# Performance work log

Hardware: AMD Instinct MI355X
Metric: run time of the kernel (lower is better)

Reference implementation:

```python
import jax, jax.numpy as jnp
import numpy as np

N_NODE = 4096
FMAPS = 64
HIDDEN = 8


def setup_inputs() -> dict:
    key = jax.random.key(0)
    k1, k2, k3, k4, k5, k6 = jax.random.split(key, 6)
    adj_in = jax.random.uniform(k1, (1, N_NODE, N_NODE), dtype=jnp.float32)
    emb_in = jax.random.normal(k2, (1, FMAPS, N_NODE), dtype=jnp.float32)
    # Linear(2*fmaps+1 -> nb_hidden) and Linear(nb_hidden -> 8), torch layout [out, in]
    W1 = jax.random.normal(k3, (HIDDEN, 2 * FMAPS + 1), dtype=jnp.float32) * 0.1
    b1 = jax.random.normal(k4, (HIDDEN,), dtype=jnp.float32) * 0.1
    W2 = jax.random.normal(k5, (8, HIDDEN), dtype=jnp.float32) * 0.1
    b2 = jax.random.normal(k6, (8,), dtype=jnp.float32) * 0.1
    return {"adj_in": adj_in, "emb_in": emb_in, "W1": W1, "b1": b1, "W2": W2, "b2": b2}


def reference(adj_in, emb_in, W1, b1, W2, b2):
    # Original module only supports batch==1 (squeeze + column assign constraint).
    batch, fmap, nb_node = emb_in.shape  # [1, F, N]
    A = adj_in[0]                        # [N, N]
    E = emb_in[0].T                      # [N, F] node embeddings

    # mean incoming edge weight per node k: (column-sum minus self edge) / (N-1)
    sum_w = (jnp.sum(A, axis=0) - jnp.diagonal(A)) / (nb_node - 1)  # [N]

    # Pairwise input for pair (j,k) is [E[j], E[k], sum_w[k]] fed through layer1.
    # Decompose layer1 linearly instead of materializing the [N*N, 2F+1] tensor.
    W1a = W1[:, :fmap]            # acts on first sample (row j)
    W1b = W1[:, fmap:2 * fmap]    # acts on second sample (col k)
    w1c = W1[:, 2 * fmap]         # acts on incoming edge weight (col k)

    aj = E @ W1a.T + b1                               # [N, H] contribution of j
    bk = E @ W1b.T + sum_w[:, None] * w1c[None, :]    # [N, H] contribution of k

    h = jax.nn.relu(aj[:, None, :] + bk[None, :, :])  # [N, N, H]
    # layer2 then keep output channel 0 only (as original scatters edge_out[:, 0])
    adj = h @ W2[0] + b2[0]                           # [N, N]
    return adj[None]                                  # [1, N, N]
```

## Files before the change

kernel.cpp:

```cpp
#include <hip/hip_runtime.h>

#define N 4096
#define F 64
#define H 8
#define PCHUNKS 256
#define W1S (2 * F + 1)

__global__ __launch_bounds__(256) void colsum_partial(const float* __restrict__ A,
                                                      float* __restrict__ partial) {
    int c4 = blockIdx.x * 256 + threadIdx.x;
    int r0 = blockIdx.y * (N / PCHUNKS);
    const float* p = A + (size_t)r0 * N + (size_t)c4 * 4;
    float4 acc = make_float4(0.f, 0.f, 0.f, 0.f);
#pragma unroll
    for (int r = 0; r < N / PCHUNKS; ++r) {
        float4 v = *(const float4*)(p + (size_t)r * N);
        acc.x += v.x; acc.y += v.y; acc.z += v.z; acc.w += v.w;
    }
    *(float4*)(partial + (size_t)blockIdx.y * N + (size_t)c4 * 4) = acc;
}

__global__ __launch_bounds__(256) void fuse_tile(const float* __restrict__ A,
                                                 const float* __restrict__ emb,
                                                 const float* __restrict__ W1,
                                                 const float* __restrict__ b1,
                                                 const float* __restrict__ W2,
                                                 const float* __restrict__ b2,
                                                 const float* __restrict__ partial,
                                                 float* __restrict__ out) {
    __shared__ float ajs[128][12];
    __shared__ float bks_s[128][12];
    __shared__ float psum[128][2];

    const int t  = threadIdx.x;
    const int j0 = blockIdx.x * 128;
    const int i0 = blockIdx.y * 128;

    {
        int c = t & 127;
        int half = t >> 7;
        const float* pp = partial + (size_t)half * 128 * N + (size_t)j0 + c;
        float s = 0.f;
#pragma unroll 16
        for (int p = 0; p < 128; ++p) s += pp[(size_t)p * N];
        psum[c][half] = s;
    }
    __syncthreads();

    if (t < 128) {
        int j = j0 + t;
        float sw = (psum[t][0] + psum[t][1] - A[(size_t)j * N + j]) * (1.0f / (float)(N - 1));
        float b[H];
#pragma unroll
        for (int k = 0; k < H; ++k) b[k] = sw * W1[k * W1S + 2 * F];
#pragma unroll
        for (int f = 0; f < F; ++f) {
            float e = emb[(size_t)f * N + j];
#pragma unroll
            for (int k = 0; k < H; ++k) b[k] += e * W1[k * W1S + F + f];
        }
#pragma unroll
        for (int k = 0; k < H; ++k) bks_s[t][k] = b[k];
    } else {
        int r = t - 128;
        int i = i0 + r;
        float a[H];
#pragma unroll
        for (int k = 0; k < H; ++k) a[k] = b1[k];
#pragma unroll
        for (int f = 0; f < F; ++f) {
            float e = emb[(size_t)f * N + i];
#pragma unroll
            for (int k = 0; k < H; ++k) a[k] += e * W1[k * W1S + f];
        }
#pragma unroll
        for (int k = 0; k < H; ++k) ajs[r][k] = a[k];
    }
    __syncthreads();

    int tx = t & 31;
    int ty = t >> 5;
    int j  = j0 + tx * 4;

    float w2[H];
#pragma unroll
    for (int k = 0; k < H; ++k) w2[k] = W2[k];
    float b20 = b2[0];

    float bkr[4][H];
#pragma unroll
    for (int c = 0; c < 4; ++c) {
        float4 lo = *(const float4*)&bks_s[tx * 4 + c][0];
        float4 hi = *(const float4*)&bks_s[tx * 4 + c][4];
        bkr[c][0] = lo.x; bkr[c][1] = lo.y; bkr[c][2] = lo.z; bkr[c][3] = lo.w;
        bkr[c][4] = hi.x; bkr[c][5] = hi.y; bkr[c][6] = hi.z; bkr[c][7] = hi.w;
    }

#pragma unroll
    for (int r = 0; r < 16; ++r) {
        int row = ty * 16 + r;
        float a[H];
        float4 lo = *(const float4*)&ajs[row][0];
        float4 hi = *(const float4*)&ajs[row][4];
        a[0] = lo.x; a[1] = lo.y; a[2] = lo.z; a[3] = lo.w;
        a[4] = hi.x; a[5] = hi.y; a[6] = hi.z; a[7] = hi.w;

        float res[4];
#pragma unroll
        for (int c = 0; c < 4; ++c) {
            float acc = b20;
#pragma unroll
            for (int k = 0; k < H; ++k) {
                float tt = a[k] + bkr[c][k];
                acc += fmaxf(tt, 0.f) * w2[k];
            }
            res[c] = acc;
        }
        *(float4*)(out + (size_t)(i0 + row) * N + j) = make_float4(res[0], res[1], res[2], res[3]);
    }
}

extern "C" void kernel_launch(void* const* d_in, const int* in_sizes, int n_in,
                              void* d_out, int out_size, void* d_ws, size_t ws_size,
                              hipStream_t stream) {
    const float* adj = (const float*)d_in[0];
    const float* emb = (const float*)d_in[1];
    const float* W1  = (const float*)d_in[2];
    const float* b1  = (const float*)d_in[3];
    const float* W2  = (const float*)d_in[4];
    const float* b2  = (const float*)d_in[5];
    float* out = (float*)d_out;

    float* partial = (float*)d_ws;

    colsum_partial<<<dim3(4, PCHUNKS), 256, 0, stream>>>(adj, partial);
    fuse_tile<<<dim3(N / 128, N / 128), 256, 0, stream>>>(adj, emb, W1, b1, W2, b2,
                                                          partial, out);
}
```

Before: 40.80 us.

## Fuse column-sum and pairwise MLP into one kernel with per-stripe atomic barrier

Merges the column-sum pass into the main kernel. Each block reduces a 256x128 tile of A, writes a partial, then spins on a per-column-stripe atomic counter until all 16 row bands have contributed. Blocks now cover 256 output rows, so the aj projection is computed for two rows per thread. This removes one launch and the 256-chunk partial buffer but adds a memset, a grid-wide spin wait that relies on all 512 blocks being co-resident, and a serialized reduction before any output is written.

```diff
diff --git a/kernel.cpp b/kernel.cpp
--- a/kernel.cpp
+++ b/kernel.cpp
@@ -3,120 +3,145 @@
 #define N 4096
 #define F 64
 #define H 8
-#define PCHUNKS 256
 #define W1S (2 * F + 1)
+#define NSTRIPE 32
+#define NBAND 16
 
-__global__ __launch_bounds__(256) void colsum_partial(const float* __restrict__ A,
-                                                      float* __restrict__ partial) {
-    int c4 = blockIdx.x * 256 + threadIdx.x;
-    int r0 = blockIdx.y * (N / PCHUNKS);
-    const float* p = A + (size_t)r0 * N + (size_t)c4 * 4;
-    float4 acc = make_float4(0.f, 0.f, 0.f, 0.f);
-#pragma unroll
-    for (int r = 0; r < N / PCHUNKS; ++r) {
-        float4 v = *(const float4*)(p + (size_t)r * N);
-        acc.x += v.x; acc.y += v.y; acc.z += v.z; acc.w += v.w;
-    }
-    *(float4*)(partial + (size_t)blockIdx.y * N + (size_t)c4 * 4) = acc;
-}
-
-__global__ __launch_bounds__(256) void fuse_tile(const float* __restrict__ A,
-                                                 const float* __restrict__ emb,
-                                                 const float* __restrict__ W1,
-                                                 const float* __restrict__ b1,
-                                                 const float* __restrict__ W2,
-                                                 const float* __restrict__ b2,
-                                                 const float* __restrict__ partial,
-                                                 float* __restrict__ out) {
-    __shared__ float ajs[128][12];
-    __shared__ float bks_s[128][12];
-    __shared__ float psum[128][2];
+__global__ __launch_bounds__(256, 2) void fused_all(
+    const float* __restrict__ A, const float* __restrict__ emb,
+    const float* __restrict__ W1, const float* __restrict__ b1,
+    const float* __restrict__ W2, const float* __restrict__ b2,
+    unsigned* __restrict__ cnt, float* __restrict__ partial,
+    float* __restrict__ out)
+{
+    __shared__ float4 ps[8][32];
+    __shared__ float ajs[256][12];
+    __shared__ float bks[128][12];
 
     const int t  = threadIdx.x;
-    const int j0 = blockIdx.x * 128;
-    const int i0 = blockIdx.y * 128;
+    const int s  = blockIdx.x >> 4;
+    const int rb = blockIdx.x & 15;
+    const int j0 = s * 128;
+    const int i0 = rb * 256;
 
     {
-        int c = t & 127;
-        int half = t >> 7;
-        const float* pp = partial + (size_t)half * 128 * N + (size_t)j0 + c;
-        float s = 0.f;
+        int c4 = t & 31;
+        int rg = t >> 5;
+        const float* p = A + (size_t)(i0 + rg * 32) * N + j0 + c4 * 4;
+        float4 acc = make_float4(0.f, 0.f, 0.f, 0.f);
 #pragma unroll 16
-        for (int p = 0; p < 128; ++p) s += pp[(size_t)p * N];
-        psum[c][half] = s;
+        for (int r = 0; r < 32; ++r) {
+            float4 v = *(const float4*)(p + (size_t)r * N);
+            acc.x += v.x; acc.y += v.y; acc.z += v.z; acc.w += v.w;
+        }
+        ps[rg][c4] = acc;
+    }
+    __syncthreads();
+    if (t < 32) {
+        float4 tot = make_float4(0.f, 0.f, 0.f, 0.f);
+#pragma unroll
+        for (int g = 0; g < 8; ++g) {
+            float4 v = ps[g][t];
+            tot.x += v.x; tot.y += v.y; tot.z += v.z; tot.w += v.w;
+        }
+        *(float4*)(partial + (size_t)blockIdx.x * 128 + t * 4) = tot;
+    }
+    __syncthreads();
+
+    if (t == 0) {
+        __threadfence();
+        atomicAdd(&cnt[s], 1u);
+        while (__hip_atomic_load(&cnt[s], __ATOMIC_RELAXED,
+                                 __HIP_MEMORY_SCOPE_AGENT) < (unsigned)NBAND) {
+            __builtin_amdgcn_s_sleep(16);
+        }
+        __threadfence();
     }
     __syncthreads();
 
     if (t < 128) {
+        float tot = 0.f;
+#pragma unroll
+        for (int r = 0; r < NBAND; ++r)
+            tot += partial[(size_t)(s * NBAND + r) * 128 + t];
         int j = j0 + t;
-        float sw = (psum[t][0] + psum[t][1] - A[(size_t)j * N + j]) * (1.0f / (float)(N - 1));
-        float b[H];
+        float sw = (tot - A[(size_t)j * N + j]) * (1.0f / (float)(N - 1));
+        float bv[H];
 #pragma unroll
-        for (int k = 0; k < H; ++k) b[k] = sw * W1[k * W1S + 2 * F];
+        for (int k = 0; k < H; ++k) bv[k] = sw * W1[k * W1S + 2 * F];
 #pragma unroll
         for (int f = 0; f < F; ++f) {
             float e = emb[(size_t)f * N + j];
 #pragma unroll
-            for (int k = 0; k < H; ++k) b[k] += e * W1[k * W1S + F + f];
+            for (int k = 0; k < H; ++k) bv[k] += e * W1[k * W1S + F + f];
         }
 #pragma unroll
-        for (int k = 0; k < H; ++k) bks_s[t][k] = b[k];
+        for (int k = 0; k < H; ++k) bks[t][k] = bv[k];
     } else {
-        int r = t - 128;
-        int i = i0 + r;
-        float a[H];
+        int u = t - 128;
+        float a0[H], a1[H];
 #pragma unroll
-        for (int k = 0; k < H; ++k) a[k] = b1[k];
+        for (int k = 0; k < H; ++k) { a0[k] = b1[k]; a1[k] = b1[k]; }
 #pragma unroll
         for (int f = 0; f < F; ++f) {
-            float e = emb[(size_t)f * N + i];
+            float e0 = emb[(size_t)f * N + i0 + u];
+            float e1 = emb[(size_t)f * N + i0 + 128 + u];
 #pragma unroll
-            for (int k = 0; k < H; ++k) a[k] += e * W1[k * W1S + f];
+            for (int k = 0; k < H; ++k) {
+                a0[k] += e0 * W1[k * W1S + f];
+                a1[k] += e1 * W1[k * W1S + f];
+            }
         }
 #pragma unroll
-        for (int k = 0; k < H; ++k) ajs[r][k] = a[k];
+        for (int k = 0; k < H; ++k) { ajs[u][k] = a0[k]; ajs[128 + u][k] = a1[k]; }
     }
     __syncthreads();
 
-    int tx = t & 31;
-    int ty = t >> 5;
-    int j  = j0 + tx * 4;
+    {
+        int tx = t & 31;
+        int ty = t >> 5;
+        int j  = j0 + tx * 4;
 
-    float w2[H];
+        float w2[H];
 #pragma unroll
-    for (int k = 0; k < H; ++k) w2[k] = W2[k];
-    float b20 = b2[0];
+        for (int k = 0; k < H; ++k) w2[k] = W2[k];
+        float b20 = b2[0];
 
-    float bkr[4][H];
-#pragma unroll
-    for (int c = 0; c < 4; ++c) {
-        float4 lo = *(const float4*)&bks_s[tx * 4 + c][0];
-        float4 hi = *(const float4*)&bks_s[tx * 4 + c][4];
-        bkr[c][0] = lo.x; bkr[c][1] = lo.y; bkr[c][2] = lo.z; bkr[c][3] = lo.w;
-        bkr[c][4] = hi.x; bkr[c][5] = hi.y; bkr[c][6] = hi.z; bkr[c][7] = hi.w;
-    }
-
-#pragma unroll
-    for (int r = 0; r < 16; ++r) {
-        int row = ty * 16 + r;
-        float a[H];
-        float4 lo = *(const float4*)&ajs[row][0];
-        float4 hi = *(const float4*)&ajs[row][4];
-        a[0] = lo.x; a[1] = lo.y; a[2] = lo.z; a[3] = lo.w;
-        a[4] = hi.x; a[5] = hi.y; a[6] = hi.z; a[7] = hi.w;
-
-        float res[4];
+        float bkr[4][H];
 #pragma unroll
         for (int c = 0; c < 4; ++c) {
-            float acc = b20;
+            float4 lo = *(const float4*)&bks[tx * 4 + c][0];
+            float4 hi = *(const float4*)&bks[tx * 4 + c][4];
+            bkr[c][0] = lo.x; bkr[c][1] = lo.y; bkr[c][2] = lo.z; bkr[c][3] = lo.w;
+            bkr[c][4] = hi.x; bkr[c][5] = hi.y; bkr[c][6] = hi.z; bkr[c][7] = hi.w;
+        }
+
+#pragma unroll 2
+        for (int half = 0; half < 2; ++half) {
 #pragma unroll
-            for (int k = 0; k < H; ++k) {
-                float tt = a[k] + bkr[c][k];
-                acc += fmaxf(tt, 0.f) * w2[k];
+            for (int r = 0; r < 16; ++r) {
+                int row = half * 128 + ty * 16 + r;
+                float a[H];
+                float4 lo = *(const float4*)&ajs[row][0];
+                float4 hi = *(const float4*)&ajs[row][4];
+                a[0] = lo.x; a[1] = lo.y; a[2] = lo.z; a[3] = lo.w;
+                a[4] = hi.x; a[5] = hi.y; a[6] = hi.z; a[7] = hi.w;
+
+                float res[4];
+#pragma unroll
+                for (int c = 0; c < 4; ++c) {
+                    float acc = b20;
+#pragma unroll
+                    for (int k = 0; k < H; ++k) {
+                        float tt = a[k] + bkr[c][k];
+                        acc += fmaxf(tt, 0.f) * w2[k];
+                    }
+                    res[c] = acc;
+                }
+                *(float4*)(out + (size_t)(i0 + row) * N + j) =
+                    make_float4(res[0], res[1], res[2], res[3]);
             }
-            res[c] = acc;
         }
-        *(float4*)(out + (size_t)(i0 + row) * N + j) = make_float4(res[0], res[1], res[2], res[3]);
     }
 }
 
@@ -131,9 +156,10 @@
     const float* b2  = (const float*)d_in[5];
     float* out = (float*)d_out;
 
-    float* partial = (float*)d_ws;
+    unsigned* cnt  = (unsigned*)d_ws;
+    float* partial = (float*)((char*)d_ws + 512);
 
-    colsum_partial<<<dim3(4, PCHUNKS), 256, 0, stream>>>(adj, partial);
-    fuse_tile<<<dim3(N / 128, N / 128), 256, 0, stream>>>(adj, emb, W1, b1, W2, b2,
-                                                          partial, out);
+    hipMemsetAsync(d_ws, 0, 512, stream);
+    fused_all<<<dim3(NSTRIPE * NBAND), 256, 0, stream>>>(adj, emb, W1, b1, W2, b2,
+                                                         cnt, partial, out);
 }
```

New measurement: 90.22 us. 2.21x slower.

## Widen output tile to 256 columns and halve column-sum partial chunks

Applied to the files above, without the earlier changes.

The column-sum pre-pass now uses 128 row chunks of 32 rows instead of 256 chunks of 16, which halves the partial buffer each tile must re-read. The main kernel tile grows to 128x256, so every thread computes one column's bk vector directly from its own partial sum, without the shared-memory reduction and its extra barrier. Each thread also writes 32 rows instead of 16. This cuts redundant per-tile recomputation of bk and aj and the partial-sum rereads, at the cost of fewer blocks and more per-thread serial work.

```diff
diff --git a/kernel.cpp b/kernel.cpp
--- a/kernel.cpp
+++ b/kernel.cpp
@@ -3,17 +3,17 @@
 #define N 4096
 #define F 64
 #define H 8
-#define PCHUNKS 256
 #define W1S (2 * F + 1)
+#define PCH 128
 
 __global__ __launch_bounds__(256) void colsum_partial(const float* __restrict__ A,
                                                       float* __restrict__ partial) {
     int c4 = blockIdx.x * 256 + threadIdx.x;
-    int r0 = blockIdx.y * (N / PCHUNKS);
+    int r0 = blockIdx.y * 32;
     const float* p = A + (size_t)r0 * N + (size_t)c4 * 4;
     float4 acc = make_float4(0.f, 0.f, 0.f, 0.f);
-#pragma unroll
-    for (int r = 0; r < N / PCHUNKS; ++r) {
+#pragma unroll 16
+    for (int r = 0; r < 32; ++r) {
         float4 v = *(const float4*)(p + (size_t)r * N);
         acc.x += v.x; acc.y += v.y; acc.z += v.z; acc.w += v.w;
     }
@@ -29,57 +29,53 @@
                                                  const float* __restrict__ partial,
                                                  float* __restrict__ out) {
     __shared__ float ajs[128][12];
-    __shared__ float bks_s[128][12];
-    __shared__ float psum[128][2];
+    __shared__ float bks[256][12];
 
     const int t  = threadIdx.x;
-    const int j0 = blockIdx.x * 128;
+    const int j0 = blockIdx.x * 256;
     const int i0 = blockIdx.y * 128;
 
+    float s = 0.f;
     {
-        int c = t & 127;
-        int half = t >> 7;
-        const float* pp = partial + (size_t)half * 128 * N + (size_t)j0 + c;
-        float s = 0.f;
+        const float* pp = partial + j0 + t;
 #pragma unroll 16
-        for (int p = 0; p < 128; ++p) s += pp[(size_t)p * N];
-        psum[c][half] = s;
+        for (int p = 0; p < PCH; ++p) s += pp[(size_t)p * N];
     }
-    __syncthreads();
 
-    if (t < 128) {
+    {
         int j = j0 + t;
-        float sw = (psum[t][0] + psum[t][1] - A[(size_t)j * N + j]) * (1.0f / (float)(N - 1));
-        float b[H];
+        float sw = (s - A[(size_t)j * N + j]) * (1.0f / (float)(N - 1));
+        float bv[H];
 #pragma unroll
-        for (int k = 0; k < H; ++k) b[k] = sw * W1[k * W1S + 2 * F];
+        for (int k = 0; k < H; ++k) bv[k] = sw * W1[k * W1S + 2 * F];
 #pragma unroll
         for (int f = 0; f < F; ++f) {
             float e = emb[(size_t)f * N + j];
 #pragma unroll
-            for (int k = 0; k < H; ++k) b[k] += e * W1[k * W1S + F + f];
+            for (int k = 0; k < H; ++k) bv[k] += e * W1[k * W1S + F + f];
         }
 #pragma unroll
-        for (int k = 0; k < H; ++k) bks_s[t][k] = b[k];
-    } else {
-        int r = t - 128;
-        int i = i0 + r;
-        float a[H];
+        for (int k = 0; k < H; ++k) bks[t][k] = bv[k];
+    }
+
+    if (t < 128) {
+        int i = i0 + t;
+        float av[H];
 #pragma unroll
-        for (int k = 0; k < H; ++k) a[k] = b1[k];
+        for (int k = 0; k < H; ++k) av[k] = b1[k];
 #pragma unroll
         for (int f = 0; f < F; ++f) {
             float e = emb[(size_t)f * N + i];
 #pragma unroll
-            for (int k = 0; k < H; ++k) a[k] += e * W1[k * W1S + f];
+            for (int k = 0; k < H; ++k) av[k] += e * W1[k * W1S + f];
         }
 #pragma unroll
-        for (int k = 0; k < H; ++k) ajs[r][k] = a[k];
+        for (int k = 0; k < H; ++k) ajs[t][k] = av[k];
     }
     __syncthreads();
 
-    int tx = t & 31;
-    int ty = t >> 5;
+    int tx = t & 63;
+    int ty = t >> 6;
     int j  = j0 + tx * 4;
 
     float w2[H];
@@ -90,15 +86,15 @@
     float bkr[4][H];
 #pragma unroll
     for (int c = 0; c < 4; ++c) {
-        float4 lo = *(const float4*)&bks_s[tx * 4 + c][0];
-        float4 hi = *(const float4*)&bks_s[tx * 4 + c][4];
+        float4 lo = *(const float4*)&bks[tx * 4 + c][0];
+        float4 hi = *(const float4*)&bks[tx * 4 + c][4];
         bkr[c][0] = lo.x; bkr[c][1] = lo.y; bkr[c][2] = lo.z; bkr[c][3] = lo.w;
         bkr[c][4] = hi.x; bkr[c][5] = hi.y; bkr[c][6] = hi.z; bkr[c][7] = hi.w;
     }
 
 #pragma unroll
-    for (int r = 0; r < 16; ++r) {
-        int row = ty * 16 + r;
+    for (int r = 0; r < 32; ++r) {
+        int row = ty * 32 + r;
         float a[H];
         float4 lo = *(const float4*)&ajs[row][0];
         float4 hi = *(const float4*)&ajs[row][4];
@@ -116,7 +112,8 @@
             }
             res[c] = acc;
         }
-        *(float4*)(out + (size_t)(i0 + row) * N + j) = make_float4(res[0], res[1], res[2], res[3]);
+        *(float4*)(out + (size_t)(i0 + row) * N + j) =
+            make_float4(res[0], res[1], res[2], res[3]);
     }
 }
 
@@ -133,7 +130,7 @@
 
     float* partial = (float*)d_ws;
 
-    colsum_partial<<<dim3(4, PCHUNKS), 256, 0, stream>>>(adj, partial);
-    fuse_tile<<<dim3(N / 128, N / 128), 256, 0, stream>>>(adj, emb, W1, b1, W2, b2,
+    colsum_partial<<<dim3(4, PCH), 256, 0, stream>>>(adj, partial);
+    fuse_tile<<<dim3(N / 256, N / 128), 256, 0, stream>>>(adj, emb, W1, b1, W2, b2,
                                                           partial, out);
 }
```

Result: slower. 50.22 us (+23.1%).
